# Kernel tuning notes

Hardware: AMD Instinct MI355X
Metric: run time of the kernel (lower is better)

Reference implementation:

```python
import jax, jax.numpy as jnp
import numpy as np

EMB = 256
HID = 256
NH = 8
HD = HID // NH  # 32
EPS = 1e-5


def _wn(v, g):
    # torch weight_norm(dim=0): per-output-row normalization of v
    return g[:, None] * v / jnp.linalg.norm(v, axis=1, keepdims=True)


def _ln(x, gamma, beta):
    mu = jnp.mean(x, axis=-1, keepdims=True)
    var = jnp.mean((x - mu) ** 2, axis=-1, keepdims=True)
    return (x - mu) * jax.lax.rsqrt(var + EPS) * gamma + beta


def _rope(x):
    # x: [B', S, H, D]; torchtune-style rotary embedding, base 10000
    S, D = x.shape[1], x.shape[3]
    freqs = 1.0 / (10000.0 ** (jnp.arange(0, D, 2, dtype=jnp.float32) / D))  # [D/2]
    ang = jnp.arange(S, dtype=jnp.float32)[:, None] * freqs[None, :]          # [S, D/2]
    cos = jnp.cos(ang)[None, :, None, :]
    sin = jnp.sin(ang)[None, :, None, :]
    xr = x.reshape(*x.shape[:-1], D // 2, 2)
    x0, x1 = xr[..., 0], xr[..., 1]
    out = jnp.stack([x0 * cos - x1 * sin, x1 * cos + x0 * sin], axis=-1)
    return out.reshape(x.shape)


def setup_inputs() -> dict:
    key = jax.random.key(0)
    ks = jax.random.split(key, 12)
    s = lambda shp: 0.02
    return {
        "z": jax.random.normal(ks[0], (2, 32, 512, EMB), dtype=jnp.float32),
        "ln1_g": jnp.ones((EMB,), jnp.float32),
        "ln1_b": jnp.zeros((EMB,), jnp.float32),
        "proj_v": jax.random.normal(ks[1], (3 * HID, EMB), jnp.float32) * 0.02,
        "proj_g": jnp.ones((3 * HID,), jnp.float32),
        "proj_b": jnp.zeros((3 * HID,), jnp.float32),
        "ff_v": jax.random.normal(ks[2], (EMB, HID), jnp.float32) * 0.02,
        "ff_g": jnp.ones((EMB,), jnp.float32),
        "ff_b": jnp.zeros((EMB,), jnp.float32),
        "ln2_g": jnp.ones((EMB,), jnp.float32),
        "ln2_b": jnp.zeros((EMB,), jnp.float32),
        "w1_v": jax.random.normal(ks[3], (EMB, EMB), jnp.float32) * 0.02,
        "w1_g": jnp.ones((EMB,), jnp.float32),
        "w1_b": jnp.zeros((EMB,), jnp.float32),
        "w2_v": jax.random.normal(ks[4], (EMB, EMB), jnp.float32) * 0.02,
        "w2_g": jnp.ones((EMB,), jnp.float32),
        "w2_b": jnp.zeros((EMB,), jnp.float32),
    }


def reference(z, ln1_g, ln1_b, proj_v, proj_g, proj_b, ff_v, ff_g, ff_b,
              ln2_g, ln2_b, w1_v, w1_g, w1_b, w2_v, w2_g, w2_b):
    B, U, A, E = z.shape
    BU = B * U
    Wqkv = _wn(proj_v, proj_g)   # [3H, E]
    Wo = _wn(ff_v, ff_g)         # [E, H]
    # ---- RoPE attention block ----
    z_ = _ln(z, ln1_g, ln1_b).reshape(BU, A, E)
    qkv = z_ @ Wqkv.T + proj_b                       # [BU, A, 3H]
    qkv = qkv.reshape(BU, A, NH, 3 * HD)
    q, k, v = jnp.split(qkv, 3, axis=-1)             # each [BU, A, NH, HD]
    q = _rope(q)
    k = _rope(k)
    qh = q.transpose(0, 2, 1, 3)                     # [BU, NH, A, HD]
    kh = k.transpose(0, 2, 1, 3)
    vh = v.transpose(0, 2, 1, 3)
    scores = jnp.einsum('bhqd,bhkd->bhqk', qh, kh) / jnp.sqrt(jnp.float32(HD))
    attn = jax.nn.softmax(scores, axis=-1)
    out = jnp.einsum('bhqk,bhkd->bhqd', attn, vh)    # [BU, NH, A, HD]
    out = out.transpose(0, 2, 1, 3).reshape(BU, A, HID)
    out = out @ Wo.T + ff_b
    z = z + out.reshape(B, U, A, E)
    # ---- NormFF block ----
    W1 = _wn(w1_v, w1_g)
    W2 = _wn(w2_v, w2_g)
    h = _ln(z, ln2_g, ln2_b)
    h = jax.nn.gelu(h @ W1.T + w1_b, approximate=False)
    h = h @ W2.T + w2_b
    return z + h
```

## Files before the change

### kernel.cpp

```cpp
#include <hip/hip_runtime.h>
#include <cmath>

#define EMB 256
#define NHEAD 8
#define HD 32
#define A_LEN 512
#define TOK 32768

typedef __bf16 bf16_t;
typedef __bf16 bf16x8 __attribute__((ext_vector_type(8)));
typedef __bf16 bf16x4 __attribute__((ext_vector_type(4)));
typedef float floatx4 __attribute__((ext_vector_type(4)));

#define MFMA16(a, b, c) __builtin_amdgcn_mfma_f32_16x16x32_bf16((a), (b), (c), 0, 0, 0)

__global__ __launch_bounds__(64) void setup_kernel(
    const float* __restrict__ proj_v, const float* __restrict__ proj_g,
    const float* __restrict__ ff_v, const float* __restrict__ ff_g,
    const float* __restrict__ w1_v, const float* __restrict__ w1_g,
    const float* __restrict__ w2_v, const float* __restrict__ w2_g,
    bf16_t* __restrict__ Wall, float* __restrict__ ctab,
    float* __restrict__ stab) {
    int b = blockIdx.x;
    int lane = threadIdx.x;
    if (b < 1536) {
        const float* v; const float* g; int r;
        if (b < 768)       { v = proj_v; g = proj_g; r = b; }
        else if (b < 1024) { v = ff_v;   g = ff_g;   r = b - 768; }
        else if (b < 1280) { v = w1_v;   g = w1_g;   r = b - 1024; }
        else               { v = w2_v;   g = w2_g;   r = b - 1280; }
        const floatx4* vr = (const floatx4*)(v + (size_t)r * 256);
        floatx4 x = vr[lane];
        float ss = x[0] * x[0] + x[1] * x[1] + x[2] * x[2] + x[3] * x[3];
#pragma unroll
        for (int off = 32; off >= 1; off >>= 1) ss += __shfl_xor(ss, off);
        float sc = g[r] * rsqrtf(ss);
        bf16x4 o;
        o[0] = (bf16_t)(x[0] * sc); o[1] = (bf16_t)(x[1] * sc);
        o[2] = (bf16_t)(x[2] * sc); o[3] = (bf16_t)(x[3] * sc);
        ((bf16x4*)(Wall + (size_t)b * 256))[lane] = o;
    } else {
        int idx = (b - 1536) * 64 + lane;
        int a = idx >> 4, i = idx & 15;
        float freq = expf(-(float)(2 * i) * 0.2878231366242558f);
        float ang = (float)a * freq;
        ctab[idx] = cosf(ang);
        stab[idx] = sinf(ang);
    }
}

__global__ __launch_bounds__(256, 2) void qkv_kernel(
    const float* __restrict__ z, const float* __restrict__ ln_g,
    const float* __restrict__ ln_b, const bf16_t* __restrict__ W,
    const float* __restrict__ pb, const float* __restrict__ ctab,
    const float* __restrict__ stab, bf16_t* __restrict__ qbf,
    bf16_t* __restrict__ kbf, bf16_t* __restrict__ vtb) {
    __shared__ bf16_t xns[64 * 264];
    __shared__ bf16_t vls[256 * 72];
    int tid = threadIdx.x;
    int t0 = blockIdx.x * 64;

#pragma unroll
    for (int it = 0; it < 4; ++it) {
        int row = it * 16 + (tid >> 4);
        int sub = tid & 15;
        const floatx4* zr = (const floatx4*)(z + (size_t)(t0 + row) * 256 + sub * 16);
        floatx4 v0 = zr[0], v1 = zr[1], v2 = zr[2], v3 = zr[3];
        float vals[16];
        ((floatx4*)vals)[0] = v0; ((floatx4*)vals)[1] = v1;
        ((floatx4*)vals)[2] = v2; ((floatx4*)vals)[3] = v3;
        float s = 0.f, q2 = 0.f;
#pragma unroll
        for (int i = 0; i < 16; ++i) { s += vals[i]; q2 += vals[i] * vals[i]; }
#pragma unroll
        for (int off = 8; off >= 1; off >>= 1) {
            s += __shfl_xor(s, off);
            q2 += __shfl_xor(q2, off);
        }
        float mu = s * (1.f / 256.f);
        float inv = rsqrtf(q2 * (1.f / 256.f) - mu * mu + 1e-5f);
        int cb = sub * 16;
        bf16x8 o0, o1;
#pragma unroll
        for (int i = 0; i < 8; ++i)
            o0[i] = (bf16_t)((vals[i] - mu) * inv * ln_g[cb + i] + ln_b[cb + i]);
#pragma unroll
        for (int i = 0; i < 8; ++i)
            o1[i] = (bf16_t)((vals[8 + i] - mu) * inv * ln_g[cb + 8 + i] + ln_b[cb + 8 + i]);
        *(bf16x8*)&xns[row * 264 + cb] = o0;
        *(bf16x8*)&xns[row * 264 + cb + 8] = o1;
    }
    __syncthreads();

    int wv = tid >> 6, lane = tid & 63, quad = lane >> 4, lidx = lane & 15;

    bf16x8 afr[4][8];
#pragma unroll
    for (int mt = 0; mt < 4; ++mt)
#pragma unroll
        for (int kc = 0; kc < 8; ++kc)
            afr[mt][kc] = *(const bf16x8*)&xns[(mt * 16 + lidx) * 264 + kc * 32 + quad * 8];

#pragma unroll 1
    for (int nt = 0; nt < 12; ++nt) {
        int nbase = wv * 192 + nt * 16;
        int n = nbase + lidx;
        bf16x8 bfr[8];
#pragma unroll
        for (int kc = 0; kc < 8; ++kc)
            bfr[kc] = *(const bf16x8*)&W[(size_t)n * 256 + kc * 32 + quad * 8];
        floatx4 acc[4];
#pragma unroll
        for (int mt = 0; mt < 4; ++mt) acc[mt] = (floatx4){0.f, 0.f, 0.f, 0.f};
#pragma unroll
        for (int kc = 0; kc < 8; ++kc)
#pragma unroll
            for (int mt = 0; mt < 4; ++mt)
                acc[mt] = MFMA16(afr[mt][kc], bfr[kc], acc[mt]);

        float bias = pb[n];
        int htile = nbase / 96;
        int rem = nbase % 96;
        int sec = rem >> 5;
        int d = (rem & 31) + lidx;
#pragma unroll
        for (int mt = 0; mt < 4; ++mt) {
#pragma unroll
            for (int r = 0; r < 4; ++r) {
                int tok = t0 + mt * 16 + quad * 4 + r;
                int a = tok & 511;
                int bu = tok >> 9;
                float val = acc[mt][r] + bias;
                if (sec == 2) {
                    int a_loc = mt * 16 + quad * 4 + r;
                    vls[(htile * 32 + d) * 72 + a_loc] = (bf16_t)val;
                } else {
                    size_t addr = ((size_t)((bu * 8 + htile) * 512 + a)) * 32 + d;
                    float part = __shfl_xor(val, 1);
                    float cs = ctab[a * 16 + (d >> 1)];
                    float sn = stab[a * 16 + (d >> 1)];
                    float res = ((d & 1) == 0) ? (val * cs - part * sn)
                                               : (val * cs + part * sn);
                    if (sec == 0)
                        qbf[addr] = (bf16_t)(res * 0.17677669529663687f);
                    else
                        kbf[addr] = (bf16_t)res;
                }
            }
        }
    }
    __syncthreads();
    {
        int bu = t0 >> 9, a0 = t0 & 511;
        size_t gbase = ((size_t)(bu * 256 + tid)) * 512 + a0;
#pragma unroll
        for (int j = 0; j < 8; ++j)
            *(bf16x8*)&vtb[gbase + j * 8] = *(const bf16x8*)&vls[tid * 72 + j * 8];
    }
}

__global__ __launch_bounds__(512, 4) void attn_kernel(
    const bf16_t* __restrict__ qbf, const bf16_t* __restrict__ kbf,
    const bf16_t* __restrict__ vtb, bf16_t* __restrict__ ob) {
    __shared__ bf16_t Kls[512 * 32];
    __shared__ bf16_t Vt[32 * 512];
    __shared__ bf16_t Pls[8 * 16 * 64];
    int tid = threadIdx.x;
    int wv = tid >> 6, lane = tid & 63, quad = lane >> 4, lidx = lane & 15;
    int bh = blockIdx.x;
    int bu = bh >> 3, h = bh & 7;
    size_t hb = (size_t)bh * (A_LEN * HD);

#pragma unroll
    for (int i = 0; i < 4; ++i) {
        int c = tid + i * 512;
        int key = c >> 2, blk = c & 3;
        bf16x8 kv = *(const bf16x8*)&kbf[hb + (size_t)c * 8];
        *(bf16x8*)&Kls[key * 32 + ((blk ^ (key & 3)) << 3)] = kv;
        int vrow = c >> 6, vblk = c & 63;
        bf16x8 vv = *(const bf16x8*)&vtb[hb + (size_t)c * 8];
        *(bf16x8*)&Vt[vrow * 512 + ((vblk ^ (vrow & 7)) << 3)] = vv;
    }
    __syncthreads();

    int pbase = wv * (16 * 64);
    const floatx4 cm8 = (floatx4){-8.f, -8.f, -8.f, -8.f};
    const floatx4 zero4 = (floatx4){0.f, 0.f, 0.f, 0.f};

#pragma unroll 1
    for (int mt = 0; mt < 4; ++mt) {
        int q0 = wv * 64 + mt * 16;
        bf16x8 qfrag = *(const bf16x8*)&qbf[hb + (size_t)(q0 + lidx) * 32 + quad * 8];
        float l_[4] = {0.f, 0.f, 0.f, 0.f};
        floatx4 Oacc[2];
        Oacc[0] = zero4; Oacc[1] = zero4;

#pragma unroll 1
        for (int kc = 0; kc < 8; ++kc) {
            floatx4 sc[4];
#pragma unroll
            for (int t = 0; t < 4; ++t) {
                bf16x8 kf = *(const bf16x8*)&Kls[(kc * 64 + t * 16 + lidx) * 32 +
                                                 ((quad ^ (lidx & 3)) << 3)];
                sc[t] = MFMA16(qfrag, kf, cm8);
            }
            float p[4][4];
#pragma unroll
            for (int t = 0; t < 4; ++t)
#pragma unroll
                for (int r = 0; r < 4; ++r) p[t][r] = __expf(sc[t][r]);
#pragma unroll
            for (int t = 0; t < 4; ++t)
#pragma unroll
                for (int r = 0; r < 4; ++r) {
                    int row = quad * 4 + r;
                    int pc = (t * 16 + lidx) ^ ((row & 7) << 3);
                    Pls[pbase + row * 64 + pc] = (bf16_t)p[t][r];
                }
#pragma unroll
            for (int r = 0; r < 4; ++r) {
                float s = (p[0][r] + p[1][r]) + (p[2][r] + p[3][r]);
#pragma unroll
                for (int off = 8; off >= 1; off >>= 1) s += __shfl_xor(s, off);
                l_[r] += s;
            }
#pragma unroll
            for (int ks = 0; ks < 2; ++ks) {
                bf16x8 pf = *(const bf16x8*)&Pls[pbase + lidx * 64 +
                                                 (((ks * 4 + quad) ^ (lidx & 7)) << 3)];
#pragma unroll
                for (int nt = 0; nt < 2; ++nt) {
                    int vrow = nt * 16 + lidx;
                    bf16x8 vf = *(const bf16x8*)&Vt[vrow * 512 +
                        ((kc * 8 + ((ks * 4 + quad) ^ (lidx & 7))) << 3)];
                    Oacc[nt] = MFMA16(pf, vf, Oacc[nt]);
                }
            }
        }
#pragma unroll
        for (int nt = 0; nt < 2; ++nt)
#pragma unroll
            for (int r = 0; r < 4; ++r) {
                int tok = bu * 512 + q0 + quad * 4 + r;
                ob[(size_t)tok * 256 + h * 32 + nt * 16 + lidx] =
                    (bf16_t)(Oacc[nt][r] / l_[r]);
            }
    }
}

__global__ __launch_bounds__(256, 2) void tail_kernel(
    const bf16_t* __restrict__ X, const bf16_t* __restrict__ Wo,
    const float* __restrict__ obias, const float* __restrict__ zin,
    const float* __restrict__ ln_g, const float* __restrict__ ln_b,
    const bf16_t* __restrict__ W1, const float* __restrict__ b1,
    const bf16_t* __restrict__ W2, const float* __restrict__ b2,
    float* __restrict__ outp) {
    __shared__ bf16_t xns[64 * 264];
    __shared__ bf16_t hs[64 * 264];
    __shared__ float red[64 * 8];
    __shared__ float mi[64 * 2];
    int tid = threadIdx.x;
    int t0 = blockIdx.x * 64;
    int wv = tid >> 6, lane = tid & 63, quad = lane >> 4, lidx = lane & 15;

    bf16x8 afr[4][8];
#pragma unroll
    for (int mt = 0; mt < 4; ++mt)
#pragma unroll
        for (int kc = 0; kc < 8; ++kc)
            afr[mt][kc] = *(const bf16x8*)&X[(size_t)(t0 + mt * 16 + lidx) * 256 + kc * 32 + quad * 8];

    float r1[4][4][4];
#pragma unroll 1
    for (int nt = 0; nt < 4; ++nt) {
        int n = wv * 64 + nt * 16 + lidx;
        bf16x8 bfr[8];
#pragma unroll
        for (int kc = 0; kc < 8; ++kc)
            bfr[kc] = *(const bf16x8*)&Wo[(size_t)n * 256 + kc * 32 + quad * 8];
        floatx4 acc[4];
#pragma unroll
        for (int mt = 0; mt < 4; ++mt) acc[mt] = (floatx4){0.f, 0.f, 0.f, 0.f};
#pragma unroll
        for (int kc = 0; kc < 8; ++kc)
#pragma unroll
            for (int mt = 0; mt < 4; ++mt)
                acc[mt] = MFMA16(afr[mt][kc], bfr[kc], acc[mt]);
        float b = obias[n];
#pragma unroll
        for (int mt = 0; mt < 4; ++mt)
#pragma unroll
            for (int r = 0; r < 4; ++r) {
                size_t o = (size_t)(t0 + mt * 16 + quad * 4 + r) * 256 + n;
                r1[nt][mt][r] = zin[o] + acc[mt][r] + b;
            }
    }

#pragma unroll
    for (int mt = 0; mt < 4; ++mt)
#pragma unroll
        for (int r = 0; r < 4; ++r) {
            float s = 0.f, ss = 0.f;
#pragma unroll
            for (int nt = 0; nt < 4; ++nt) {
                float v = r1[nt][mt][r];
                s += v; ss += v * v;
            }
#pragma unroll
            for (int off = 8; off >= 1; off >>= 1) {
                s += __shfl_xor(s, off);
                ss += __shfl_xor(ss, off);
            }
            if (lidx == 0) {
                int row = mt * 16 + quad * 4 + r;
                red[row * 8 + wv * 2] = s;
                red[row * 8 + wv * 2 + 1] = ss;
            }
        }
    __syncthreads();
    if (tid < 64) {
        float s = 0.f, ss = 0.f;
#pragma unroll
        for (int w = 0; w < 4; ++w) {
            s += red[tid * 8 + w * 2];
            ss += red[tid * 8 + w * 2 + 1];
        }
        float mu = s * (1.f / 256.f);
        mi[tid * 2] = mu;
        mi[tid * 2 + 1] = rsqrtf(ss * (1.f / 256.f) - mu * mu + 1e-5f);
    }
    __syncthreads();

    float gv[4], bv[4];
#pragma unroll
    for (int nt = 0; nt < 4; ++nt) {
        int n = wv * 64 + nt * 16 + lidx;
        gv[nt] = ln_g[n]; bv[nt] = ln_b[n];
    }
#pragma unroll
    for (int mt = 0; mt < 4; ++mt)
#pragma unroll
        for (int r = 0; r < 4; ++r) {
            int row = mt * 16 + quad * 4 + r;
            float mu = mi[row * 2], inv = mi[row * 2 + 1];
#pragma unroll
            for (int nt = 0; nt < 4; ++nt) {
                int n = wv * 64 + nt * 16 + lidx;
                xns[row * 264 + n] = (bf16_t)((r1[nt][mt][r] - mu) * inv * gv[nt] + bv[nt]);
            }
        }
    __syncthreads();

#pragma unroll
    for (int mt = 0; mt < 4; ++mt)
#pragma unroll
        for (int kc = 0; kc < 8; ++kc)
            afr[mt][kc] = *(const bf16x8*)&xns[(mt * 16 + lidx) * 264 + kc * 32 + quad * 8];
#pragma unroll 1
    for (int nt = 0; nt < 4; ++nt) {
        int n = wv * 64 + nt * 16 + lidx;
        bf16x8 bfr[8];
#pragma unroll
        for (int kc = 0; kc < 8; ++kc)
            bfr[kc] = *(const bf16x8*)&W1[(size_t)n * 256 + kc * 32 + quad * 8];
        floatx4 acc[4];
#pragma unroll
        for (int mt = 0; mt < 4; ++mt) acc[mt] = (floatx4){0.f, 0.f, 0.f, 0.f};
#pragma unroll
        for (int kc = 0; kc < 8; ++kc)
#pragma unroll
            for (int mt = 0; mt < 4; ++mt)
                acc[mt] = MFMA16(afr[mt][kc], bfr[kc], acc[mt]);
        float b = b1[n];
#pragma unroll
        for (int mt = 0; mt < 4; ++mt)
#pragma unroll
            for (int r = 0; r < 4; ++r) {
                float x = acc[mt][r] + b;
                float gel = 0.5f * x * (1.f + erff(x * 0.7071067811865476f));
                hs[(mt * 16 + quad * 4 + r) * 264 + n] = (bf16_t)gel;
            }
    }
    __syncthreads();

#pragma unroll
    for (int mt = 0; mt < 4; ++mt)
#pragma unroll
        for (int kc = 0; kc < 8; ++kc)
            afr[mt][kc] = *(const bf16x8*)&hs[(mt * 16 + lidx) * 264 + kc * 32 + quad * 8];
#pragma unroll 1
    for (int nt = 0; nt < 4; ++nt) {
        int n = wv * 64 + nt * 16 + lidx;
        bf16x8 bfr[8];
#pragma unroll
        for (int kc = 0; kc < 8; ++kc)
            bfr[kc] = *(const bf16x8*)&W2[(size_t)n * 256 + kc * 32 + quad * 8];
        floatx4 acc[4];
#pragma unroll
        for (int mt = 0; mt < 4; ++mt) acc[mt] = (floatx4){0.f, 0.f, 0.f, 0.f};
#pragma unroll
        for (int kc = 0; kc < 8; ++kc)
#pragma unroll
            for (int mt = 0; mt < 4; ++mt)
                acc[mt] = MFMA16(afr[mt][kc], bfr[kc], acc[mt]);
        float b = b2[n];
#pragma unroll
        for (int mt = 0; mt < 4; ++mt)
#pragma unroll
            for (int r = 0; r < 4; ++r) {
                size_t o = (size_t)(t0 + mt * 16 + quad * 4 + r) * 256 + n;
                outp[o] = r1[nt][mt][r] + acc[mt][r] + b;
            }
    }
}

extern "C" void kernel_launch(void* const* d_in, const int* in_sizes, int n_in,
                              void* d_out, int out_size, void* d_ws, size_t ws_size,
                              hipStream_t stream) {
    const float* z      = (const float*)d_in[0];
    const float* ln1_g  = (const float*)d_in[1];
    const float* ln1_b  = (const float*)d_in[2];
    const float* proj_v = (const float*)d_in[3];
    const float* proj_g = (const float*)d_in[4];
    const float* proj_b = (const float*)d_in[5];
    const float* ff_v   = (const float*)d_in[6];
    const float* ff_g   = (const float*)d_in[7];
    const float* ff_b   = (const float*)d_in[8];
    const float* ln2_g  = (const float*)d_in[9];
    const float* ln2_b  = (const float*)d_in[10];
    const float* w1_v   = (const float*)d_in[11];
    const float* w1_g   = (const float*)d_in[12];
    const float* w1_b   = (const float*)d_in[13];
    const float* w2_v   = (const float*)d_in[14];
    const float* w2_g   = (const float*)d_in[15];
    const float* w2_b   = (const float*)d_in[16];
    float* out = (float*)d_out;

    char* p = (char*)d_ws;
    bf16_t* Wall = (bf16_t*)p; p += (size_t)1536 * 256 * 2;
    float* ctab  = (float*)p;  p += 8192 * 4;
    float* stab  = (float*)p;  p += 8192 * 4;
    bf16_t* qbf  = (bf16_t*)p; p += (size_t)TOK * 256 * 2;
    bf16_t* kbf  = (bf16_t*)p; p += (size_t)TOK * 256 * 2;
    bf16_t* vtb  = (bf16_t*)p; p += (size_t)TOK * 256 * 2;
    bf16_t* abuf = (bf16_t*)p; p += (size_t)TOK * 256 * 2;

    const bf16_t* Wqkv = Wall;
    const bf16_t* Wo   = Wall + (size_t)768 * 256;
    const bf16_t* W1   = Wall + (size_t)1024 * 256;
    const bf16_t* W2   = Wall + (size_t)1280 * 256;

    setup_kernel<<<1664, 64, 0, stream>>>(proj_v, proj_g, ff_v, ff_g,
                                          w1_v, w1_g, w2_v, w2_g,
                                          Wall, ctab, stab);
    qkv_kernel<<<TOK / 64, 256, 0, stream>>>(z, ln1_g, ln1_b, Wqkv, proj_b,
                                             ctab, stab, qbf, kbf, vtb);
    attn_kernel<<<64 * 8, 512, 0, stream>>>(qbf, kbf, vtb, abuf);
    tail_kernel<<<TOK / 64, 256, 0, stream>>>(abuf, Wo, ff_b, z, ln2_g, ln2_b,
                                              W1, w1_b, W2, w2_b, out);
}
```

Before: 286.0 us.

## Double block size to 8 waves, compute softmax sums via MFMA, stage output stores

The qkv and tail kernels now launch 512 threads (8 waves) per block. Each wave takes half as many output columns, so per-wave register pressure falls and the compiler can fit more waves in flight. The attention kernel computes the softmax row sums with an extra MFMA against a ones vector instead of shuffle reductions, and unrolls the key loop by two. The tail kernel stages its final fp32 output through shared memory so global stores are coalesced 16-byte writes. The trade-offs are extra LDS traffic, an extra barrier, and bf16-rounded probabilities in the denominator sum.

```diff
diff --git a/kernel.cpp b/kernel.cpp
--- a/kernel.cpp
+++ b/kernel.cpp
@@ -49,7 +49,7 @@
     }
 }
 
-__global__ __launch_bounds__(256, 2) void qkv_kernel(
+__global__ __launch_bounds__(512, 4) void qkv_kernel(
     const float* __restrict__ z, const float* __restrict__ ln_g,
     const float* __restrict__ ln_b, const bf16_t* __restrict__ W,
     const float* __restrict__ pb, const float* __restrict__ ctab,
@@ -61,8 +61,8 @@
     int t0 = blockIdx.x * 64;
 
 #pragma unroll
-    for (int it = 0; it < 4; ++it) {
-        int row = it * 16 + (tid >> 4);
+    for (int it = 0; it < 2; ++it) {
+        int row = it * 32 + (tid >> 4);
         int sub = tid & 15;
         const floatx4* zr = (const floatx4*)(z + (size_t)(t0 + row) * 256 + sub * 16);
         floatx4 v0 = zr[0], v1 = zr[1], v2 = zr[2], v3 = zr[3];
@@ -102,9 +102,8 @@
             afr[mt][kc] = *(const bf16x8*)&xns[(mt * 16 + lidx) * 264 + kc * 32 + quad * 8];
 
 #pragma unroll 1
-    for (int nt = 0; nt < 12; ++nt) {
-        int nbase = wv * 192 + nt * 16;
-        int n = nbase + lidx;
+    for (int nt = 0; nt < 6; ++nt) {
+        int n = wv * 96 + nt * 16 + lidx;
         bf16x8 bfr[8];
 #pragma unroll
         for (int kc = 0; kc < 8; ++kc)
@@ -119,10 +118,8 @@
                 acc[mt] = MFMA16(afr[mt][kc], bfr[kc], acc[mt]);
 
         float bias = pb[n];
-        int htile = nbase / 96;
-        int rem = nbase % 96;
-        int sec = rem >> 5;
-        int d = (rem & 31) + lidx;
+        int sec = nt >> 1;
+        int d = (nt & 1) * 16 + lidx;
 #pragma unroll
         for (int mt = 0; mt < 4; ++mt) {
 #pragma unroll
@@ -133,9 +130,9 @@
                 float val = acc[mt][r] + bias;
                 if (sec == 2) {
                     int a_loc = mt * 16 + quad * 4 + r;
-                    vls[(htile * 32 + d) * 72 + a_loc] = (bf16_t)val;
+                    vls[(wv * 32 + d) * 72 + a_loc] = (bf16_t)val;
                 } else {
-                    size_t addr = ((size_t)((bu * 8 + htile) * 512 + a)) * 32 + d;
+                    size_t addr = ((size_t)((bu * 8 + wv) * 512 + a)) * 32 + d;
                     float part = __shfl_xor(val, 1);
                     float cs = ctab[a * 16 + (d >> 1)];
                     float sn = stab[a * 16 + (d >> 1)];
@@ -152,10 +149,13 @@
     __syncthreads();
     {
         int bu = t0 >> 9, a0 = t0 & 511;
-        size_t gbase = ((size_t)(bu * 256 + tid)) * 512 + a0;
-#pragma unroll
-        for (int j = 0; j < 8; ++j)
-            *(bf16x8*)&vtb[gbase + j * 8] = *(const bf16x8*)&vls[tid * 72 + j * 8];
+#pragma unroll
+        for (int ps = 0; ps < 4; ++ps) {
+            int c = ps * 512 + tid;
+            int row = c >> 3, col8 = c & 7;
+            *(bf16x8*)&vtb[((size_t)(bu * 256 + row)) * 512 + a0 + col8 * 8] =
+                *(const bf16x8*)&vls[row * 72 + col8 * 8];
+        }
     }
 }
 
@@ -186,16 +186,18 @@
     int pbase = wv * (16 * 64);
     const floatx4 cm8 = (floatx4){-8.f, -8.f, -8.f, -8.f};
     const floatx4 zero4 = (floatx4){0.f, 0.f, 0.f, 0.f};
+    bf16x8 ones;
+#pragma unroll
+    for (int j = 0; j < 8; ++j) ones[j] = (bf16_t)1.0f;
 
 #pragma unroll 1
     for (int mt = 0; mt < 4; ++mt) {
         int q0 = wv * 64 + mt * 16;
         bf16x8 qfrag = *(const bf16x8*)&qbf[hb + (size_t)(q0 + lidx) * 32 + quad * 8];
-        float l_[4] = {0.f, 0.f, 0.f, 0.f};
-        floatx4 Oacc[2];
-        Oacc[0] = zero4; Oacc[1] = zero4;
-
-#pragma unroll 1
+        floatx4 Oacc[2], lacc;
+        Oacc[0] = zero4; Oacc[1] = zero4; lacc = zero4;
+
+#pragma unroll 2
         for (int kc = 0; kc < 8; ++kc) {
             floatx4 sc[4];
 #pragma unroll
@@ -204,30 +206,20 @@
                                                  ((quad ^ (lidx & 3)) << 3)];
                 sc[t] = MFMA16(qfrag, kf, cm8);
             }
-            float p[4][4];
 #pragma unroll
             for (int t = 0; t < 4; ++t)
 #pragma unroll
-                for (int r = 0; r < 4; ++r) p[t][r] = __expf(sc[t][r]);
-#pragma unroll
-            for (int t = 0; t < 4; ++t)
-#pragma unroll
                 for (int r = 0; r < 4; ++r) {
+                    float p = __expf(sc[t][r]);
                     int row = quad * 4 + r;
                     int pc = (t * 16 + lidx) ^ ((row & 7) << 3);
-                    Pls[pbase + row * 64 + pc] = (bf16_t)p[t][r];
+                    Pls[pbase + row * 64 + pc] = (bf16_t)p;
                 }
-#pragma unroll
-            for (int r = 0; r < 4; ++r) {
-                float s = (p[0][r] + p[1][r]) + (p[2][r] + p[3][r]);
-#pragma unroll
-                for (int off = 8; off >= 1; off >>= 1) s += __shfl_xor(s, off);
-                l_[r] += s;
-            }
 #pragma unroll
             for (int ks = 0; ks < 2; ++ks) {
                 bf16x8 pf = *(const bf16x8*)&Pls[pbase + lidx * 64 +
                                                  (((ks * 4 + quad) ^ (lidx & 7)) << 3)];
+                lacc = MFMA16(pf, ones, lacc);
 #pragma unroll
                 for (int nt = 0; nt < 2; ++nt) {
                     int vrow = nt * 16 + lidx;
@@ -238,27 +230,30 @@
             }
         }
 #pragma unroll
-        for (int nt = 0; nt < 2; ++nt)
-#pragma unroll
-            for (int r = 0; r < 4; ++r) {
-                int tok = bu * 512 + q0 + quad * 4 + r;
+        for (int r = 0; r < 4; ++r) {
+            float inv = 1.f / lacc[r];
+            int tok = bu * 512 + q0 + quad * 4 + r;
+#pragma unroll
+            for (int nt = 0; nt < 2; ++nt)
                 ob[(size_t)tok * 256 + h * 32 + nt * 16 + lidx] =
-                    (bf16_t)(Oacc[nt][r] / l_[r]);
-            }
+                    (bf16_t)(Oacc[nt][r] * inv);
+        }
     }
 }
 
-__global__ __launch_bounds__(256, 2) void tail_kernel(
+__global__ __launch_bounds__(512, 4) void tail_kernel(
     const bf16_t* __restrict__ X, const bf16_t* __restrict__ Wo,
     const float* __restrict__ obias, const float* __restrict__ zin,
     const float* __restrict__ ln_g, const float* __restrict__ ln_b,
     const bf16_t* __restrict__ W1, const float* __restrict__ b1,
     const bf16_t* __restrict__ W2, const float* __restrict__ b2,
     float* __restrict__ outp) {
-    __shared__ bf16_t xns[64 * 264];
-    __shared__ bf16_t hs[64 * 264];
-    __shared__ float red[64 * 8];
+    __shared__ __align__(16) char smem[67584];
+    __shared__ float red[64 * 16];
     __shared__ float mi[64 * 2];
+    bf16_t* xns = (bf16_t*)smem;
+    bf16_t* hs  = (bf16_t*)(smem + 33792);
+    float* stage = (float*)smem;
     int tid = threadIdx.x;
     int t0 = blockIdx.x * 64;
     int wv = tid >> 6, lane = tid & 63, quad = lane >> 4, lidx = lane & 15;
@@ -270,10 +265,10 @@
         for (int kc = 0; kc < 8; ++kc)
             afr[mt][kc] = *(const bf16x8*)&X[(size_t)(t0 + mt * 16 + lidx) * 256 + kc * 32 + quad * 8];
 
-    float r1[4][4][4];
+    float r1[2][4][4];
 #pragma unroll 1
-    for (int nt = 0; nt < 4; ++nt) {
-        int n = wv * 64 + nt * 16 + lidx;
+    for (int nt = 0; nt < 2; ++nt) {
+        int n = wv * 32 + nt * 16 + lidx;
         bf16x8 bfr[8];
 #pragma unroll
         for (int kc = 0; kc < 8; ++kc)
@@ -300,12 +295,8 @@
     for (int mt = 0; mt < 4; ++mt)
 #pragma unroll
         for (int r = 0; r < 4; ++r) {
-            float s = 0.f, ss = 0.f;
-#pragma unroll
-            for (int nt = 0; nt < 4; ++nt) {
-                float v = r1[nt][mt][r];
-                s += v; ss += v * v;
-            }
+            float s = r1[0][mt][r] + r1[1][mt][r];
+            float ss = r1[0][mt][r] * r1[0][mt][r] + r1[1][mt][r] * r1[1][mt][r];
 #pragma unroll
             for (int off = 8; off >= 1; off >>= 1) {
                 s += __shfl_xor(s, off);
@@ -313,17 +304,17 @@
             }
             if (lidx == 0) {
                 int row = mt * 16 + quad * 4 + r;
-                red[row * 8 + wv * 2] = s;
-                red[row * 8 + wv * 2 + 1] = ss;
+                red[row * 16 + wv * 2] = s;
+                red[row * 16 + wv * 2 + 1] = ss;
             }
         }
     __syncthreads();
     if (tid < 64) {
         float s = 0.f, ss = 0.f;
 #pragma unroll
-        for (int w = 0; w < 4; ++w) {
-            s += red[tid * 8 + w * 2];
-            ss += red[tid * 8 + w * 2 + 1];
+        for (int w = 0; w < 8; ++w) {
+            s += red[tid * 16 + w * 2];
+            ss += red[tid * 16 + w * 2 + 1];
         }
         float mu = s * (1.f / 256.f);
         mi[tid * 2] = mu;
@@ -331,10 +322,10 @@
     }
     __syncthreads();
 
-    float gv[4], bv[4];
-#pragma unroll
-    for (int nt = 0; nt < 4; ++nt) {
-        int n = wv * 64 + nt * 16 + lidx;
+    float gv[2], bv[2];
+#pragma unroll
+    for (int nt = 0; nt < 2; ++nt) {
+        int n = wv * 32 + nt * 16 + lidx;
         gv[nt] = ln_g[n]; bv[nt] = ln_b[n];
     }
 #pragma unroll
@@ -344,8 +335,8 @@
             int row = mt * 16 + quad * 4 + r;
             float mu = mi[row * 2], inv = mi[row * 2 + 1];
 #pragma unroll
-            for (int nt = 0; nt < 4; ++nt) {
-                int n = wv * 64 + nt * 16 + lidx;
+            for (int nt = 0; nt < 2; ++nt) {
+                int n = wv * 32 + nt * 16 + lidx;
                 xns[row * 264 + n] = (bf16_t)((r1[nt][mt][r] - mu) * inv * gv[nt] + bv[nt]);
             }
         }
@@ -357,8 +348,8 @@
         for (int kc = 0; kc < 8; ++kc)
             afr[mt][kc] = *(const bf16x8*)&xns[(mt * 16 + lidx) * 264 + kc * 32 + quad * 8];
 #pragma unroll 1
-    for (int nt = 0; nt < 4; ++nt) {
-        int n = wv * 64 + nt * 16 + lidx;
+    for (int nt = 0; nt < 2; ++nt) {
+        int n = wv * 32 + nt * 16 + lidx;
         bf16x8 bfr[8];
 #pragma unroll
         for (int kc = 0; kc < 8; ++kc)
@@ -389,8 +380,8 @@
         for (int kc = 0; kc < 8; ++kc)
             afr[mt][kc] = *(const bf16x8*)&hs[(mt * 16 + lidx) * 264 + kc * 32 + quad * 8];
 #pragma unroll 1
-    for (int nt = 0; nt < 4; ++nt) {
-        int n = wv * 64 + nt * 16 + lidx;
+    for (int nt = 0; nt < 2; ++nt) {
+        int n = wv * 32 + nt * 16 + lidx;
         bf16x8 bfr[8];
 #pragma unroll
         for (int kc = 0; kc < 8; ++kc)
@@ -407,10 +398,27 @@
 #pragma unroll
         for (int mt = 0; mt < 4; ++mt)
 #pragma unroll
-            for (int r = 0; r < 4; ++r) {
-                size_t o = (size_t)(t0 + mt * 16 + quad * 4 + r) * 256 + n;
-                outp[o] = r1[nt][mt][r] + acc[mt][r] + b;
-            }
+            for (int r = 0; r < 4; ++r)
+                r1[nt][mt][r] += acc[mt][r] + b;
+    }
+    __syncthreads();
+
+#pragma unroll
+    for (int mt = 0; mt < 4; ++mt)
+#pragma unroll
+        for (int r = 0; r < 4; ++r) {
+            int row = mt * 16 + quad * 4 + r;
+#pragma unroll
+            for (int nt = 0; nt < 2; ++nt)
+                stage[row * 260 + wv * 32 + nt * 16 + lidx] = r1[nt][mt][r];
+        }
+    __syncthreads();
+#pragma unroll
+    for (int ps = 0; ps < 8; ++ps) {
+        int c = ps * 512 + tid;
+        int row = c >> 6, c4 = c & 63;
+        floatx4 v = *(const floatx4*)&stage[row * 260 + c4 * 4];
+        *(floatx4*)&outp[(size_t)(t0 + row) * 256 + c4 * 4] = v;
     }
 }
 
@@ -453,9 +461,9 @@
     setup_kernel<<<1664, 64, 0, stream>>>(proj_v, proj_g, ff_v, ff_g,
                                           w1_v, w1_g, w2_v, w2_g,
                                           Wall, ctab, stab);
-    qkv_kernel<<<TOK / 64, 256, 0, stream>>>(z, ln1_g, ln1_b, Wqkv, proj_b,
+    qkv_kernel<<<TOK / 64, 512, 0, stream>>>(z, ln1_g, ln1_b, Wqkv, proj_b,
                                              ctab, stab, qbf, kbf, vtb);
     attn_kernel<<<64 * 8, 512, 0, stream>>>(qbf, kbf, vtb, abuf);
-    tail_kernel<<<TOK / 64, 256, 0, stream>>>(abuf, Wo, ff_b, z, ln2_g, ln2_b,
+    tail_kernel<<<TOK / 64, 512, 0, stream>>>(abuf, Wo, ff_b, z, ln2_g, ln2_b,
                                               W1, w1_b, W2, w2_b, out);
 }
```

Result: slower. 410.4 us (+43.5%).
